# Performance work log

Hardware: AMD Instinct MI355X
Metric: run time of the kernel (lower is better)

The kernel has to match this reference:

```python
import jax, jax.numpy as jnp
import numpy as np

N_HEADS = 24
ROPE_BASE = 10000.0


def apply_rope(x, offset):
    """x: (B, H, L, Dh). Rotate pairs per RoPE (Su et al., 2021)."""
    B, H, L, Dh = x.shape
    inv_freq = 1.0 / (ROPE_BASE ** (jnp.arange(0, Dh, 2, dtype=jnp.float32) / Dh))  # (Dh/2,)
    t = jnp.arange(L, dtype=jnp.float32) + offset                                   # (L,)
    freqs = jnp.outer(t, inv_freq)                                                  # (L, Dh/2)
    emb = jnp.concatenate([freqs, freqs], axis=-1)                                  # (L, Dh)
    cos = jnp.cos(emb).astype(x.dtype)
    sin = jnp.sin(emb).astype(x.dtype)
    x1, x2 = x[..., : Dh // 2], x[..., Dh // 2 :]
    rotated = jnp.concatenate([-x2, x1], axis=-1)
    return x * cos + rotated * sin


def setup_inputs() -> dict:
    key = jax.random.key(0)
    k1, k2, k3 = jax.random.split(key, 3)
    B, L, D = 4, 2048, 1536
    x = jax.random.normal(k1, (B, L, D), dtype=jnp.float32)
    # Linear weights, torch convention (out_features, in_features), scaled init
    w_qkv = jax.random.normal(k2, (3 * D, D), dtype=jnp.float32) * 0.02
    w_out = jax.random.normal(k3, (D, D), dtype=jnp.float32) * 0.02
    return {"x": x, "w_qkv": w_qkv, "w_out": w_out, "pos_offset": 0}


def reference(x, w_qkv, w_out, pos_offset):
    B, L, D = x.shape
    H = N_HEADS
    Dh = D // H
    # fused QKV projection (no bias)
    qkv = jnp.einsum('bld,ed->ble', x, w_qkv)              # (B, L, 3D)
    qkv = qkv.reshape(B, L, 3, H, Dh)
    q = qkv[:, :, 0].transpose(0, 2, 1, 3)                 # (B, H, L, Dh)
    k = qkv[:, :, 1].transpose(0, 2, 1, 3)
    v = qkv[:, :, 2].transpose(0, 2, 1, 3)
    q = apply_rope(q, pos_offset)
    k = apply_rope(k, pos_offset)
    scale = 1.0 / np.sqrt(Dh)
    scores = jnp.einsum('bhqd,bhkd->bhqk', q, k) * scale   # (B, H, L, L)
    causal = jnp.tril(jnp.ones((L, L), dtype=bool))
    scores = jnp.where(causal, scores, jnp.finfo(scores.dtype).min)
    attn = jax.nn.softmax(scores, axis=-1)
    out = jnp.einsum('bhqk,bhkd->bhqd', attn, v)           # (B, H, L, Dh)
    out = out.transpose(0, 2, 1, 3).reshape(B, L, D)
    return jnp.einsum('bld,ed->ble', out, w_out)           # (B, L, D)
```

## Files before the change

### kernel.cpp

```cpp
#include <hip/hip_runtime.h>
#include <hip/hip_bf16.h>
#include <math.h>

typedef unsigned short u16;
typedef __bf16 b8 __attribute__((ext_vector_type(8)));
typedef __bf16 bf2t __attribute__((ext_vector_type(2)));
typedef float f4 __attribute__((ext_vector_type(4)));

#define B_ 4
#define L_ 2048
#define D_ 1536
#define H_ 24
#define DH_ 64

__device__ __forceinline__ float bf2f(u16 v) {
    union { unsigned u; float f; } z; z.u = ((unsigned)v) << 16; return z.f;
}
__device__ __forceinline__ u16 f2bf(float f) {
    union { float f; unsigned u; } z; z.f = f;
    unsigned u = z.u;
    return (u16)((u + 0x7fffu + ((u >> 16) & 1u)) >> 16);
}
__device__ __forceinline__ void f4_to_bf4(f4 v, u16 o[4]) {
#if __has_builtin(__builtin_amdgcn_cvt_pk_bf16_f32)
    union { bf2t b; unsigned u; } z0, z1;
    z0.b = __builtin_amdgcn_cvt_pk_bf16_f32(v[0], v[1]);
    z1.b = __builtin_amdgcn_cvt_pk_bf16_f32(v[2], v[3]);
    o[0] = (u16)(z0.u & 0xffffu); o[1] = (u16)(z0.u >> 16);
    o[2] = (u16)(z1.u & 0xffffu); o[3] = (u16)(z1.u >> 16);
#else
    o[0] = f2bf(v[0]); o[1] = f2bf(v[1]); o[2] = f2bf(v[2]); o[3] = f2bf(v[3]);
#endif
}

__global__ __launch_bounds__(256) void cvt_f32_bf16(const float* __restrict__ src,
                                                    u16* __restrict__ dst, int n4) {
    int i = blockIdx.x * 256 + threadIdx.x;
    if (i >= n4) return;
    float4 vv = ((const float4*)src)[i];
    f4 v = {vv.x, vv.y, vv.z, vv.w};
    u16 o4[4];
    f4_to_bf4(v, o4);
    ushort4 o = {o4[0], o4[1], o4[2], o4[3]};
    ((ushort4*)dst)[i] = o;
}


__device__ __forceinline__ void stage_half(const u16* __restrict__ G, int Kd,
                                           int row0, int k0, char* region, int tid) {
#pragma unroll
    for (int q = 0; q < 2; q++) {
        const int p = (q * 512 + tid) * 16;
        const int l = p ^ (((p >> 9) & 1) << 5);
        const int grow = row0 + (l >> 11) * 16 + ((l >> 6) & 15);
        const int gcol = k0 + (((((l >> 10) & 1) << 6) + (l & 63)) >> 1);
        __builtin_amdgcn_global_load_lds(
            (const __attribute__((address_space(1))) void*)(G + (size_t)grow * Kd + gcol),
            (__attribute__((address_space(3))) void*)(region + p), 16, 0, 0);
    }
}

template <int BUF, int MH>
__device__ __forceinline__ void lda(const char* ldsb, int wm, int lo, b8 (&aR)[4][2]) {
#pragma unroll
    for (int i = 0; i < 4; i++)
#pragma unroll
        for (int ks = 0; ks < 2; ks++)
            aR[i][ks] = *(const b8*)(ldsb + BUF * 32768 + wm * 16384 +
                                     ((MH * 4 + i) * 2 + ks) * 1024 + lo);
}
template <int BUF, int NH>
__device__ __forceinline__ void ldb(const char* ldsb, int wn, int lo, b8 (&bR)[4][2]) {
#pragma unroll
    for (int j = 0; j < 2; j++)
#pragma unroll
        for (int ks = 0; ks < 2; ks++)
            bR[NH * 2 + j][ks] = *(const b8*)(ldsb + 65536 + BUF * 32768 + (wn >> 1) * 16384 +
                                              (((wn & 1) * 4 + NH * 2 + j) * 2 + ks) * 1024 + lo);
}
template <int MH, int NH>
__device__ __forceinline__ void mfma16(b8 (&aR)[4][2], b8 (&bR)[4][2], f4 (&acc)[8][4]) {
    __builtin_amdgcn_s_setprio(1);
#pragma unroll
    for (int ks = 0; ks < 2; ks++)
#pragma unroll
        for (int i = 0; i < 4; i++)
#pragma unroll
            for (int j = 0; j < 2; j++)
                acc[MH * 4 + i][NH * 2 + j] = __builtin_amdgcn_mfma_f32_16x16x32_bf16(
                    aR[i][ks], bR[NH * 2 + j][ks], acc[MH * 4 + i][NH * 2 + j], 0, 0, 0);
    __builtin_amdgcn_s_setprio(0);
}

__global__ __launch_bounds__(512, 2) void gemm256(const u16* __restrict__ A,
                                                  const u16* __restrict__ B,
                                                  float* __restrict__ Cf,
                                                  u16* __restrict__ Qp,
                                                  u16* __restrict__ Kp,
                                                  u16* __restrict__ Vp,
                                                  int M, int N, int K, int mode) {
    __shared__ uint4 ldsv[131072 / 16];
    char* ldsb = (char*)ldsv;
    const int tid = threadIdx.x;
    const int wave = tid >> 6, lane = tid & 63;
    const int m16 = lane & 15, quad = lane >> 4;
    const int wm = wave >> 2, wn = wave & 3;
    const int bm = blockIdx.y * 256, bn = blockIdx.x * 256;
    int lo = m16 * 64 + quad * 16;
    lo ^= (m16 & 8) << 2;

    char* const As0 = ldsb;
    char* const As1 = ldsb + 32768;
    char* const Bs0 = ldsb + 65536;
    char* const Bs1 = ldsb + 98304;

    f4 acc[8][4];
#pragma unroll
    for (int i = 0; i < 8; i++)
#pragma unroll
        for (int j = 0; j < 4; j++) acc[i][j] = (f4)0.0f;

    b8 aR[4][2], bR[4][2];

    stage_half(A, K, bm, 0, As0, tid);
    stage_half(A, K, bm + 128, 0, As0 + 16384, tid);
    stage_half(B, K, bn, 0, Bs0, tid);
    stage_half(B, K, bn + 128, 0, Bs0 + 16384, tid);
    stage_half(B, K, bn, 64, Bs1, tid);
    stage_half(A, K, bm, 64, As1, tid);
    asm volatile("s_waitcnt vmcnt(4)" ::: "memory");
    __builtin_amdgcn_s_barrier();
    __builtin_amdgcn_sched_barrier(0);

    const int NIT = K >> 7;
#pragma unroll 1
    for (int it = 0; it < NIT; ++it) {
        const bool more = (it + 1 < NIT);
        const int k1 = (2 * it + 1) << 6;
        const int k2 = (2 * it + 2) << 6;
        const int k3 = (2 * it + 3) << 6;

        lda<0, 0>(ldsb, wm, lo, aR);
        ldb<0, 0>(ldsb, wn, lo, bR);
        stage_half(A, K, bm + 128, k1, As1 + 16384, tid);
        __builtin_amdgcn_s_barrier();
        mfma16<0, 0>(aR, bR, acc);
        __builtin_amdgcn_s_barrier();

        ldb<0, 1>(ldsb, wn, lo, bR);
        stage_half(B, K, bn + 128, k1, Bs1 + 16384, tid);
        __builtin_amdgcn_s_barrier();
        mfma16<0, 1>(aR, bR, acc);
        __builtin_amdgcn_s_barrier();

        lda<0, 1>(ldsb, wm, lo, aR);
        if (more) stage_half(B, K, bn, k2, Bs0, tid);
        __builtin_amdgcn_s_barrier();
        mfma16<1, 0>(aR, bR, acc);
        __builtin_amdgcn_s_barrier();

        if (more) {
            stage_half(B, K, bn + 128, k2, Bs0 + 16384, tid);
            asm volatile("s_waitcnt vmcnt(4)" ::: "memory");
        } else {
            asm volatile("s_waitcnt vmcnt(0)" ::: "memory");
        }
        __builtin_amdgcn_s_barrier();
        __builtin_amdgcn_sched_barrier(0);
        mfma16<1, 1>(aR, bR, acc);
        __builtin_amdgcn_s_barrier();

        lda<1, 0>(ldsb, wm, lo, aR);
        ldb<1, 0>(ldsb, wn, lo, bR);
        if (more) stage_half(A, K, bm, k2, As0, tid);
        __builtin_amdgcn_s_barrier();
        mfma16<0, 0>(aR, bR, acc);
        __builtin_amdgcn_s_barrier();

        ldb<1, 1>(ldsb, wn, lo, bR);
        if (more) stage_half(A, K, bm + 128, k2, As0 + 16384, tid);
        __builtin_amdgcn_s_barrier();
        mfma16<0, 1>(aR, bR, acc);
        __builtin_amdgcn_s_barrier();

        lda<1, 1>(ldsb, wm, lo, aR);
        if (more) stage_half(B, K, bn, k3, Bs1, tid);
        __builtin_amdgcn_s_barrier();
        mfma16<1, 0>(aR, bR, acc);
        __builtin_amdgcn_s_barrier();

        if (more) {
            stage_half(A, K, bm, k3, As1, tid);
            asm volatile("s_waitcnt vmcnt(4)" ::: "memory");
        } else {
            asm volatile("s_waitcnt vmcnt(0)" ::: "memory");
        }
        __builtin_amdgcn_s_barrier();
        __builtin_amdgcn_sched_barrier(0);
        mfma16<1, 1>(aR, bR, acc);
        __builtin_amdgcn_s_barrier();
    }

    if (mode == 0) {
#pragma unroll
        for (int i = 0; i < 8; i++) {
            const int row = bm + wm * 128 + i * 16 + quad * 4;
#pragma unroll
            for (int j = 0; j < 4; j++) {
                const int col = bn + wn * 64 + j * 16 + m16;
#pragma unroll
                for (int r = 0; r < 4; r++)
                    Cf[(size_t)(row + r) * N + col] = acc[i][j][r];
            }
        }
    } else {
#pragma unroll
        for (int j = 0; j < 4; j++) {
            const int colbase = bn + wn * 64 + j * 16;
            const int s = colbase / D_;
            const int h = (colbase % D_) / DH_;
            const int dh0 = (colbase % DH_) + m16;
            u16* dst = (s == 0) ? Qp : ((s == 1) ? Kp : Vp);
#pragma unroll
            for (int i = 0; i < 8; i++) {
                u16 o4[4];
                f4_to_bf4(acc[i][j], o4);
                const int row = bm + wm * 128 + i * 16 + quad * 4;
#pragma unroll
                for (int r = 0; r < 4; r++) {
                    const int rr = row + r;
                    const int b = rr >> 11, l = rr & (L_ - 1);
                    dst[((size_t)(b * H_ + h) * L_ + l) * DH_ + dh0] = o4[r];
                }
            }
        }
    }
}

__global__ __launch_bounds__(256) void rope_inplace(u16* __restrict__ Qp,
                                                    u16* __restrict__ Kp,
                                                    const int* __restrict__ pos) {
    unsigned idx = blockIdx.x * 256 + threadIdx.x;
    int i = idx & 31;
    unsigned t1 = idx >> 5;
    int l = t1 & (L_ - 1);
    unsigned t2 = t1 >> 11;
    int h = t2 % H_;
    int b = t2 / H_;
    float t = (float)(l + pos[0]);
    float invf = powf(10000.0f, -(float)(2 * i) * (1.0f / 64.0f));
    float ang = t * invf;
    float c = cosf(ang), s = sinf(ang);
    size_t base = ((size_t)(b * H_ + h) * L_ + l) * DH_;
    {
        float x1 = bf2f(Qp[base + i]), x2 = bf2f(Qp[base + i + 32]);
        Qp[base + i] = f2bf((x1 * c - x2 * s) * 0.125f);
        Qp[base + i + 32] = f2bf((x2 * c + x1 * s) * 0.125f);
    }
    {
        float x1 = bf2f(Kp[base + i]), x2 = bf2f(Kp[base + i + 32]);
        Kp[base + i] = f2bf(x1 * c - x2 * s);
        Kp[base + i + 32] = f2bf(x2 * c + x1 * s);
    }
}

__global__ __launch_bounds__(256, 3) void attn(const u16* __restrict__ Q,
                                               const u16* __restrict__ K,
                                               const u16* __restrict__ V,
                                               u16* __restrict__ O) {
    __shared__ u16 Ks[64 * 72];
    __shared__ u16 Vs[64 * 72];
    __shared__ u16 Ps[4][32 * 72];
    const int tid = threadIdx.x;
    const int wave = tid >> 6, lane = tid & 63;
    const int m16 = lane & 15, quad = lane >> 4;
    const int bh = blockIdx.y;
    const int tA = blockIdx.x;
    const int tB = 15 - tA;
    const int qA = tA * 128 + wave * 32;
    const int qB = tB * 128 + wave * 32;
    const int srow = tid >> 2, scol = (tid & 3) * 16, g = (tid & 3);

    b8 qfA[2][2], qfB[2][2];
#pragma unroll
    for (int i = 0; i < 2; i++) {
        const u16* qa = Q + ((size_t)bh * L_ + qA + i * 16 + m16) * DH_;
        qfA[i][0] = *(const b8*)(qa + quad * 8);
        qfA[i][1] = *(const b8*)(qa + 32 + quad * 8);
        const u16* qb = Q + ((size_t)bh * L_ + qB + i * 16 + m16) * DH_;
        qfB[i][0] = *(const b8*)(qb + quad * 8);
        qfB[i][1] = *(const b8*)(qb + 32 + quad * 8);
    }

    float lrA[2][4], lrB[2][4];
    f4 oaccA[2][4], oaccB[2][4];
#pragma unroll
    for (int i = 0; i < 2; i++)
#pragma unroll
        for (int r = 0; r < 4; r++) { lrA[i][r] = 0.0f; lrB[i][r] = 0.0f; }
#pragma unroll
    for (int i = 0; i < 2; i++)
#pragma unroll
        for (int n = 0; n < 4; n++) { oaccA[i][n] = (f4)0.0f; oaccB[i][n] = (f4)0.0f; }

    u16* pw = Ps[wave];

    auto process = [&](int qw, b8 (&qf)[2][2], float (&lrow)[2][4], f4 (&oacc)[2][4],
                       int kbase) {
        const bool need_mask = (kbase + 64 > qw);
        f4 s[2][4];
#pragma unroll
        for (int sub = 0; sub < 4; sub++) {
            b8 k0 = *(const b8*)(Ks + (sub * 16 + m16) * 72 + quad * 8);
            b8 k1 = *(const b8*)(Ks + (sub * 16 + m16) * 72 + 32 + quad * 8);
#pragma unroll
            for (int i = 0; i < 2; i++) {
                f4 c = (f4)0.0f;
                c = __builtin_amdgcn_mfma_f32_16x16x32_bf16(qf[i][0], k0, c, 0, 0, 0);
                c = __builtin_amdgcn_mfma_f32_16x16x32_bf16(qf[i][1], k1, c, 0, 0, 0);
                s[i][sub] = c;
            }
        }
        if (need_mask) {
#pragma unroll
            for (int i = 0; i < 2; i++)
#pragma unroll
                for (int sub = 0; sub < 4; sub++)
#pragma unroll
                    for (int r = 0; r < 4; r++) {
                        const int key = kbase + sub * 16 + m16;
                        const int qg = qw + i * 16 + quad * 4 + r;
                        float p = __expf(s[i][sub][r]);
                        p = (key <= qg) ? p : 0.0f;
                        s[i][sub][r] = p;
                        lrow[i][r] += p;
                    }
        } else {
#pragma unroll
            for (int i = 0; i < 2; i++)
#pragma unroll
                for (int sub = 0; sub < 4; sub++)
#pragma unroll
                    for (int r = 0; r < 4; r++) {
                        float p = __expf(s[i][sub][r]);
                        s[i][sub][r] = p;
                        lrow[i][r] += p;
                    }
        }
#pragma unroll
        for (int i = 0; i < 2; i++)
#pragma unroll
            for (int sub = 0; sub < 4; sub++) {
                u16 o4[4];
                f4_to_bf4(s[i][sub], o4);
#pragma unroll
                for (int r = 0; r < 4; r++)
                    pw[(i * 16 + quad * 4 + r) * 72 + sub * 16 + m16] = o4[r];
            }
#pragma unroll
        for (int ks = 0; ks < 2; ks++) {
            b8 pf[2];
#pragma unroll
            for (int i = 0; i < 2; i++)
                pf[i] = *(const b8*)(pw + (i * 16 + m16) * 72 + ks * 32 + quad * 8);
#pragma unroll
            for (int n = 0; n < 4; n++) {
                b8 vf = *(const b8*)(Vs + (n * 16 + m16) * 72 +
                                     ((ks * 32 + quad * 8 + n * 16) & 63));
#pragma unroll
                for (int i = 0; i < 2; i++)
                    oacc[i][n] = __builtin_amdgcn_mfma_f32_16x16x32_bf16(pf[i], vf, oacc[i][n], 0, 0, 0);
            }
        }
    };

    const int nkt = 2 * tB + 2;
    for (int kt = 0; kt < nkt; kt++) {
        const int kbase = kt * 64;
        __syncthreads();
        {
            const u16* kg = K + ((size_t)bh * L_ + kbase + srow) * DH_ + scol;
            uint4 a0 = *(const uint4*)kg;
            uint4 a1 = *(const uint4*)(kg + 8);
            const u16* vg = V + ((size_t)bh * L_ + kbase + srow) * DH_ + scol;
            uint4 b0 = *(const uint4*)vg;
            uint4 b1 = *(const uint4*)(vg + 8);
            *(uint4*)(Ks + srow * 72 + scol) = a0;
            *(uint4*)(Ks + srow * 72 + scol + 8) = a1;
            u16 tmp[16];
            *(uint4*)(tmp) = b0;
            *(uint4*)(tmp + 8) = b1;
#pragma unroll
            for (int e = 0; e < 16; e++)
                Vs[(scol + e) * 72 + ((srow + g * 16) & 63)] = tmp[e];
        }
        __syncthreads();
        if (kbase <= qA + 31) process(qA, qfA, lrA, oaccA, kbase);
        if (kbase <= qB + 31) process(qB, qfB, lrB, oaccB, kbase);
    }

#pragma unroll
    for (int x = 1; x < 16; x <<= 1)
#pragma unroll
        for (int i = 0; i < 2; i++)
#pragma unroll
            for (int r = 0; r < 4; r++) {
                lrA[i][r] += __shfl_xor(lrA[i][r], x, 64);
                lrB[i][r] += __shfl_xor(lrB[i][r], x, 64);
            }
    const int b = bh / H_, h = bh % H_;
#pragma unroll
    for (int i = 0; i < 2; i++)
#pragma unroll
        for (int r = 0; r < 4; r++) {
            const float invA = 1.0f / lrA[i][r];
            const float invB = 1.0f / lrB[i][r];
            const int qa = qA + i * 16 + quad * 4 + r;
            const int qb = qB + i * 16 + quad * 4 + r;
#pragma unroll
            for (int n = 0; n < 4; n++) {
                O[((size_t)(b * L_ + qa)) * D_ + h * 64 + n * 16 + m16] = f2bf(oaccA[i][n][r] * invA);
                O[((size_t)(b * L_ + qb)) * D_ + h * 64 + n * 16 + m16] = f2bf(oaccB[i][n][r] * invB);
            }
        }
}

extern "C" void kernel_launch(void* const* d_in, const int* in_sizes, int n_in,
                              void* d_out, int out_size, void* d_ws, size_t ws_size,
                              hipStream_t stream) {
    const float* x = (const float*)d_in[0];
    const float* w_qkv = (const float*)d_in[1];
    const float* w_out = (const float*)d_in[2];
    const int* pos = (const int*)d_in[3];
    float* out = (float*)d_out;

    const size_t nx = (size_t)B_ * L_ * D_;
    const size_t nwq = (size_t)3 * D_ * D_;
    const size_t nwo = (size_t)D_ * D_;
    const size_t per = (size_t)B_ * H_ * L_ * DH_;

    u16* xb = (u16*)d_ws;
    u16* wqkvb = xb + nx;
    u16* woutb = wqkvb + nwq;
    u16* Qp = woutb + nwo;
    u16* Kp = Qp + per;
    u16* Vp = Kp + per;
    u16* aO = xb;

    cvt_f32_bf16<<<(int)((nx / 4 + 255) / 256), 256, 0, stream>>>(x, xb, (int)(nx / 4));
    cvt_f32_bf16<<<(int)((nwq / 4 + 255) / 256), 256, 0, stream>>>(w_qkv, wqkvb, (int)(nwq / 4));
    cvt_f32_bf16<<<(int)((nwo / 4 + 255) / 256), 256, 0, stream>>>(w_out, woutb, (int)(nwo / 4));

    gemm256<<<dim3(3 * D_ / 256, B_ * L_ / 256), 512, 0, stream>>>(
        xb, wqkvb, nullptr, Qp, Kp, Vp, B_ * L_, 3 * D_, D_, 1);
    rope_inplace<<<(B_ * H_ * L_ * 32) / 256, 256, 0, stream>>>(Qp, Kp, pos);
    attn<<<dim3(L_ / 256, B_ * H_), 256, 0, stream>>>(Qp, Kp, Vp, aO);
    gemm256<<<dim3(D_ / 256, B_ * L_ / 256), 512, 0, stream>>>(
        aO, woutb, out, nullptr, nullptr, nullptr, B_ * L_, D_, D_, 0);
}
```

Measured before the change: 503.6 us.

## Fuse RoPE into QKV GEMM epilogue, swizzle workgroup order, pin LDS waits

The rotary embedding and the Q scaling move into the QKV GEMM epilogue, which removes the separate rope_inplace kernel and its extra read/write pass over Q and K. Both GEMM and attention workgroup indices are remapped with an XCD-style swizzle so neighbouring tiles share the L2 cache. Explicit lgkmcnt(0) waits with sched barriers are inserted before each MFMA group so LDS loads complete in a fixed order. The epilogue now evaluates powf, sinf and cosf per element inside the GEMM, which adds register pressure, and the extra waits may reduce overlap.

Result: slower. 616.8 us (+22.5%).

```diff
diff --git a/kernel.cpp b/kernel.cpp
--- a/kernel.cpp
+++ b/kernel.cpp
@@ -92,12 +92,17 @@
     __builtin_amdgcn_s_setprio(0);
 }
 
+#define LGKM_PIN() do { \
+    asm volatile("s_waitcnt lgkmcnt(0)" ::: "memory"); \
+    __builtin_amdgcn_sched_barrier(0); } while (0)
+
 __global__ __launch_bounds__(512, 2) void gemm256(const u16* __restrict__ A,
                                                   const u16* __restrict__ B,
                                                   float* __restrict__ Cf,
                                                   u16* __restrict__ Qp,
                                                   u16* __restrict__ Kp,
                                                   u16* __restrict__ Vp,
+                                                  const int* __restrict__ pos,
                                                   int M, int N, int K, int mode) {
     __shared__ uint4 ldsv[131072 / 16];
     char* ldsb = (char*)ldsv;
@@ -105,7 +110,13 @@
     const int wave = tid >> 6, lane = tid & 63;
     const int m16 = lane & 15, quad = lane >> 4;
     const int wm = wave >> 2, wn = wave & 3;
-    const int bm = blockIdx.y * 256, bn = blockIdx.x * 256;
+
+    const int gx = gridDim.x;
+    const int nwg = gx * gridDim.y;
+    const int orig = blockIdx.y * gx + blockIdx.x;
+    const int swz = (orig & 7) * (nwg >> 3) + (orig >> 3);
+    const int bm = (swz / gx) * 256, bn = (swz % gx) * 256;
+
     int lo = m16 * 64 + quad * 16;
     lo ^= (m16 & 8) << 2;
 
@@ -144,18 +155,21 @@
         ldb<0, 0>(ldsb, wn, lo, bR);
         stage_half(A, K, bm + 128, k1, As1 + 16384, tid);
         __builtin_amdgcn_s_barrier();
+        LGKM_PIN();
         mfma16<0, 0>(aR, bR, acc);
         __builtin_amdgcn_s_barrier();
 
         ldb<0, 1>(ldsb, wn, lo, bR);
         stage_half(B, K, bn + 128, k1, Bs1 + 16384, tid);
         __builtin_amdgcn_s_barrier();
+        LGKM_PIN();
         mfma16<0, 1>(aR, bR, acc);
         __builtin_amdgcn_s_barrier();
 
         lda<0, 1>(ldsb, wm, lo, aR);
         if (more) stage_half(B, K, bn, k2, Bs0, tid);
         __builtin_amdgcn_s_barrier();
+        LGKM_PIN();
         mfma16<1, 0>(aR, bR, acc);
         __builtin_amdgcn_s_barrier();
 
@@ -174,18 +188,21 @@
         ldb<1, 0>(ldsb, wn, lo, bR);
         if (more) stage_half(A, K, bm, k2, As0, tid);
         __builtin_amdgcn_s_barrier();
+        LGKM_PIN();
         mfma16<0, 0>(aR, bR, acc);
         __builtin_amdgcn_s_barrier();
 
         ldb<1, 1>(ldsb, wn, lo, bR);
         if (more) stage_half(A, K, bm + 128, k2, As0 + 16384, tid);
         __builtin_amdgcn_s_barrier();
+        LGKM_PIN();
         mfma16<0, 1>(aR, bR, acc);
         __builtin_amdgcn_s_barrier();
 
         lda<1, 1>(ldsb, wm, lo, aR);
         if (more) stage_half(B, K, bn, k3, Bs1, tid);
         __builtin_amdgcn_s_barrier();
+        LGKM_PIN();
         mfma16<1, 0>(aR, bR, acc);
         __builtin_amdgcn_s_barrier();
 
@@ -214,53 +231,59 @@
             }
         }
     } else {
-#pragma unroll
-        for (int j = 0; j < 4; j++) {
-            const int colbase = bn + wn * 64 + j * 16;
-            const int s = colbase / D_;
-            const int h = (colbase % D_) / DH_;
-            const int dh0 = (colbase % DH_) + m16;
-            u16* dst = (s == 0) ? Qp : ((s == 1) ? Kp : Vp);
-#pragma unroll
-            for (int i = 0; i < 8; i++) {
-                u16 o4[4];
-                f4_to_bf4(acc[i][j], o4);
-                const int row = bm + wm * 128 + i * 16 + quad * 4;
-#pragma unroll
-                for (int r = 0; r < 4; r++) {
-                    const int rr = row + r;
-                    const int b = rr >> 11, l = rr & (L_ - 1);
-                    dst[((size_t)(b * H_ + h) * L_ + l) * DH_ + dh0] = o4[r];
+        const int colbase0 = bn + wn * 64;
+        const int s = colbase0 / D_;
+        const int h = (colbase0 % D_) / DH_;
+        u16* dst = (s == 0) ? Qp : ((s == 1) ? Kp : Vp);
+        const int rowb = bm + wm * 128;
+        const int bidx = rowb >> 11;
+        const int l0 = rowb & (L_ - 1);
+        u16* dsth = dst + (size_t)(bidx * H_ + h) * L_ * DH_;
+        if (s == 2) {
+#pragma unroll
+            for (int j = 0; j < 4; j++) {
+                const int dh0 = j * 16 + m16;
+#pragma unroll
+                for (int i = 0; i < 8; i++) {
+                    u16 o4[4];
+                    f4_to_bf4(acc[i][j], o4);
+                    const int lr = l0 + i * 16 + quad * 4;
+#pragma unroll
+                    for (int r = 0; r < 4; r++)
+                        dsth[(size_t)(lr + r) * DH_ + dh0] = o4[r];
                 }
             }
-        }
-    }
-}
-
-__global__ __launch_bounds__(256) void rope_inplace(u16* __restrict__ Qp,
-                                                    u16* __restrict__ Kp,
-                                                    const int* __restrict__ pos) {
-    unsigned idx = blockIdx.x * 256 + threadIdx.x;
-    int i = idx & 31;
-    unsigned t1 = idx >> 5;
-    int l = t1 & (L_ - 1);
-    unsigned t2 = t1 >> 11;
-    int h = t2 % H_;
-    int b = t2 / H_;
-    float t = (float)(l + pos[0]);
-    float invf = powf(10000.0f, -(float)(2 * i) * (1.0f / 64.0f));
-    float ang = t * invf;
-    float c = cosf(ang), s = sinf(ang);
-    size_t base = ((size_t)(b * H_ + h) * L_ + l) * DH_;
-    {
-        float x1 = bf2f(Qp[base + i]), x2 = bf2f(Qp[base + i + 32]);
-        Qp[base + i] = f2bf((x1 * c - x2 * s) * 0.125f);
-        Qp[base + i + 32] = f2bf((x2 * c + x1 * s) * 0.125f);
-    }
-    {
-        float x1 = bf2f(Kp[base + i]), x2 = bf2f(Kp[base + i + 32]);
-        Kp[base + i] = f2bf(x1 * c - x2 * s);
-        Kp[base + i + 32] = f2bf(x2 * c + x1 * s);
+        } else {
+            const float qs = (s == 0) ? 0.125f : 1.0f;
+            const int p0 = pos[0];
+#pragma unroll
+            for (int j2 = 0; j2 < 2; j2++) {
+                const int ip = j2 * 16 + m16;
+                const float invf = powf(10000.0f, -(float)(2 * ip) * (1.0f / 64.0f));
+#pragma unroll
+                for (int i = 0; i < 8; i++) {
+                    const int lr = l0 + i * 16 + quad * 4;
+                    const f4 x1 = acc[i][j2], x2 = acc[i][j2 + 2];
+                    f4 y1, y2;
+#pragma unroll
+                    for (int r = 0; r < 4; r++) {
+                        const float ang = (float)(lr + r + p0) * invf;
+                        const float c = cosf(ang), sn = sinf(ang);
+                        y1[r] = (x1[r] * c - x2[r] * sn) * qs;
+                        y2[r] = (x2[r] * c + x1[r] * sn) * qs;
+                    }
+                    u16 o1[4], o2[4];
+                    f4_to_bf4(y1, o1);
+                    f4_to_bf4(y2, o2);
+#pragma unroll
+                    for (int r = 0; r < 4; r++) {
+                        const size_t base = (size_t)(lr + r) * DH_ + m16;
+                        dsth[base + j2 * 16] = o1[r];
+                        dsth[base + j2 * 16 + 32] = o2[r];
+                    }
+                }
+            }
+        }
     }
 }
 
@@ -274,8 +297,11 @@
     const int tid = threadIdx.x;
     const int wave = tid >> 6, lane = tid & 63;
     const int m16 = lane & 15, quad = lane >> 4;
-    const int bh = blockIdx.y;
-    const int tA = blockIdx.x;
+
+    const int orig = blockIdx.y * 8 + blockIdx.x;
+    const int swzb = (orig & 7) * 96 + (orig >> 3);
+    const int tA = swzb & 7;
+    const int bh = swzb >> 3;
     const int tB = 15 - tA;
     const int qA = tA * 128 + wave * 32;
     const int qB = tB * 128 + wave * 32;
@@ -452,9 +478,8 @@
     cvt_f32_bf16<<<(int)((nwo / 4 + 255) / 256), 256, 0, stream>>>(w_out, woutb, (int)(nwo / 4));
 
     gemm256<<<dim3(3 * D_ / 256, B_ * L_ / 256), 512, 0, stream>>>(
-        xb, wqkvb, nullptr, Qp, Kp, Vp, B_ * L_, 3 * D_, D_, 1);
-    rope_inplace<<<(B_ * H_ * L_ * 32) / 256, 256, 0, stream>>>(Qp, Kp, pos);
+        xb, wqkvb, nullptr, Qp, Kp, Vp, pos, B_ * L_, 3 * D_, D_, 1);
     attn<<<dim3(L_ / 256, B_ * H_), 256, 0, stream>>>(Qp, Kp, Vp, aO);
     gemm256<<<dim3(D_ / 256, B_ * L_ / 256), 512, 0, stream>>>(
-        aO, woutb, out, nullptr, nullptr, nullptr, B_ * L_, D_, D_, 0);
-}
+        aO, woutb, out, nullptr, nullptr, nullptr, pos, B_ * L_, D_, D_, 0);
+}
```
